# Performance work log

Hardware: AMD Instinct MI355X
Metric: run time of the kernel (lower is better)

## Reference

```python
import jax, jax.numpy as jnp
import numpy as np

N = 131072        # minibatch nodes
T = 100000        # rows per featured type table
D = 512           # raw feature dim for featured types
E = 256           # embedding size
NUM_NODES = 262144  # total nodes in graph (node embedding table rows)


def setup_inputs() -> dict:
    key = jax.random.key(0)
    ks = jax.random.split(key, 8)
    return {
        "node_ids": jax.random.randint(ks[0], (N,), 0, NUM_NODES),
        "node_tids": jax.random.randint(ks[1], (N,), 0, 4),
        "type_ids": jax.random.randint(ks[2], (N,), 0, T),
        "feats0": jax.random.normal(ks[3], (T, D), dtype=jnp.float32),
        "feats1": jax.random.normal(ks[4], (T, D), dtype=jnp.float32),
        "W0": jax.random.normal(ks[5], (D, E), dtype=jnp.float32) * (6.0 / (D + E)) ** 0.5,
        "W1": jax.random.normal(ks[6], (D, E), dtype=jnp.float32) * (6.0 / (D + E)) ** 0.5,
        "node_emb": jax.random.uniform(ks[7], (NUM_NODES, E), dtype=jnp.float32, minval=-1.0, maxval=1.0),
    }


def reference(node_ids, node_tids, type_ids, feats0, feats1, W0, W1, node_emb):
    # Per-type dispatch: types 0,1 have raw features projected by W_t;
    # types 2,3 read the learnable node-embedding table.
    m0 = (node_tids == 0)
    m1 = (node_tids == 1)
    # safe gather indices (masked-out rows read row 0, then zeroed)
    y0 = (feats0[jnp.where(m0, type_ids, 0)] @ W0) * m0[:, None].astype(W0.dtype)
    y1 = (feats1[jnp.where(m1, type_ids, 0)] @ W1) * m1[:, None].astype(W1.dtype)
    m_emb = jnp.logical_not(m0 | m1)
    ye = node_emb[node_ids] * m_emb[:, None].astype(node_emb.dtype)
    return y0 + y1 + ye  # [N, E]
```

## Files before the change

### kernel.cpp

```cpp
#include <hip/hip_runtime.h>
#include <hip/hip_bf16.h>

typedef __attribute__((ext_vector_type(4))) float f32x4;
typedef __attribute__((ext_vector_type(8))) short bf16x8;

#define NN 131072
#define TT 100000
#define DD 512
#define EE 256

__device__ inline ushort f2bf(float f) {
    union { float f; unsigned u; } x; x.f = f;
    unsigned r = x.u + 0x7fffu + ((x.u >> 16) & 1u);
    return (ushort)(r >> 16);
}

__global__ void compact_kernel(const int* __restrict__ tids, int* __restrict__ cnt,
                               int* __restrict__ l0, int* __restrict__ l1) {
    const int i = blockIdx.x * 256 + threadIdx.x;
    const int t = tids[i];
    const int lane = threadIdx.x & 63, wid = threadIdx.x >> 6;
    unsigned long long b0 = __ballot(t == 0);
    unsigned long long b1 = __ballot(t == 1);
    __shared__ int w0[4], w1[4];
    __shared__ int base0, base1;
    if (lane == 0) { w0[wid] = __popcll(b0); w1[wid] = __popcll(b1); }
    __syncthreads();
    if (threadIdx.x == 0) {
        base0 = atomicAdd(&cnt[0], w0[0] + w0[1] + w0[2] + w0[3]);
        base1 = atomicAdd(&cnt[1], w1[0] + w1[1] + w1[2] + w1[3]);
    }
    __syncthreads();
    int p0 = 0, p1 = 0;
#pragma unroll
    for (int w = 0; w < 4; ++w) if (w < wid) { p0 += w0[w]; p1 += w1[w]; }
    const unsigned long long ltm = (1ull << lane) - 1ull;
    if (t == 0)      l0[base0 + p0 + __popcll(b0 & ltm)] = i;
    else if (t == 1) l1[base1 + p1 + __popcll(b1 & ltm)] = i;
}

__global__ void prep_w_kernel(const float* __restrict__ W0, const float* __restrict__ W1,
                              ushort* __restrict__ Wt0, ushort* __restrict__ Wt1,
                              int* __restrict__ cnt) {
    if (blockIdx.x == 0 && threadIdx.x < 4) cnt[threadIdx.x] = 0;
    int gid = blockIdx.x * 256 + threadIdx.x;
    int t = gid >> 15;
    int rem = gid & 32767;
    int d = rem >> 6, eg = rem & 63;
    const float* W = t ? W1 : W0;
    ushort* Wt = t ? Wt1 : Wt0;
    f32x4 v = *(const f32x4*)(W + d * EE + eg * 4);
#pragma unroll
    for (int j = 0; j < 4; ++j)
        Wt[(size_t)(eg * 4 + j) * DD + d] = f2bf(v[j]);
}

__global__ void emb_gather_kernel(const int* __restrict__ ids, const int* __restrict__ tids,
                                  const float* __restrict__ emb, float* __restrict__ out) {
    int gid = blockIdx.x * 256 + threadIdx.x;
    int i = gid >> 6, j = gid & 63;
    if (tids[i] >= 2) {
        ((f32x4*)out)[(size_t)i * 64 + j] = ((const f32x4*)emb)[(size_t)ids[i] * 64 + j];
    }
}

__global__ __launch_bounds__(512, 4) void gemm_gather_kernel(
    const int* __restrict__ l0, const int* __restrict__ l1,
    const int* __restrict__ cntp, const int* __restrict__ type_ids,
    const float* __restrict__ feats0, const float* __restrict__ feats1,
    const ushort* __restrict__ Wt0, const ushort* __restrict__ Wt1,
    float* __restrict__ out) {
    const int cnt0 = cntp[0], cnt1 = cntp[1];
    const int ntile0 = (cnt0 + 127) >> 7;
    const int ntile1 = (cnt1 + 127) >> 7;
    const int b = blockIdx.x;
    const int* list; const float* feats; const ushort* Wt; int cnt, tile;
    if (b < ntile0)                { tile = b;          list = l0; feats = feats0; Wt = Wt0; cnt = cnt0; }
    else if (b < ntile0 + ntile1)  { tile = b - ntile0; list = l1; feats = feats1; Wt = Wt1; cnt = cnt1; }
    else return;
    const int row0 = tile * 128;

    __shared__ char Alds[128 * 64 * 2];
    __shared__ char Blds[256 * 64 * 2];

    const int tid = threadIdx.x;
    const int lane = tid & 63, wid = tid >> 6;
    const int wr = wid >> 1, wc = wid & 1;
    const int ln15 = lane & 15, lq = lane >> 4;

    const int ar = tid >> 2, aseg = tid & 3;
    const int rg = row0 + ar;
    int arow = 0;
    if (rg < cnt) arow = type_ids[list[rg]];
    const float* asrc = feats + (size_t)arow * DD + aseg * 16;
    int aw0 = ar * 128 + aseg * 32;
    int aw1 = aw0 + 16;
    aw0 ^= (ar & 7) << 4;
    aw1 ^= (ar & 7) << 4;

    f32x4 acc[2][8] = {};

    for (int k0 = 0; k0 < DD; k0 += 64) {
        const f32x4* ap = (const f32x4*)(asrc + k0);
        f32x4 v0 = ap[0], v1 = ap[1], v2 = ap[2], v3 = ap[3];
        bf16x8 h0, h1;
        h0[0] = (short)f2bf(v0[0]); h0[1] = (short)f2bf(v0[1]);
        h0[2] = (short)f2bf(v0[2]); h0[3] = (short)f2bf(v0[3]);
        h0[4] = (short)f2bf(v1[0]); h0[5] = (short)f2bf(v1[1]);
        h0[6] = (short)f2bf(v1[2]); h0[7] = (short)f2bf(v1[3]);
        h1[0] = (short)f2bf(v2[0]); h1[1] = (short)f2bf(v2[1]);
        h1[2] = (short)f2bf(v2[2]); h1[3] = (short)f2bf(v2[3]);
        h1[4] = (short)f2bf(v3[0]); h1[5] = (short)f2bf(v3[1]);
        h1[6] = (short)f2bf(v3[2]); h1[7] = (short)f2bf(v3[3]);
        *(bf16x8*)(Alds + aw0) = h0;
        *(bf16x8*)(Alds + aw1) = h1;

#pragma unroll
        for (int p = 0; p < 4; ++p) {
            int c = p * 512 + tid;
            int col = c >> 3, seg = c & 7;
            bf16x8 bv = *(const bf16x8*)(Wt + col * DD + k0 + seg * 8);
            int addr = col * 128 + seg * 16;
            addr ^= (col & 7) << 4;
            *(bf16x8*)(Blds + addr) = bv;
        }
        __syncthreads();

#pragma unroll
        for (int kh = 0; kh < 2; ++kh) {
            const int kb = kh * 64 + lq * 16;
            int ra0 = wr * 32 + ln15;
            int a0addr = (ra0 * 128 + kb) ^ ((ra0 & 7) << 4);
            int ra1 = ra0 + 16;
            int a1addr = (ra1 * 128 + kb) ^ ((ra1 & 7) << 4);
            bf16x8 a0 = *(const bf16x8*)(Alds + a0addr);
            bf16x8 a1 = *(const bf16x8*)(Alds + a1addr);
#pragma unroll
            for (int ni = 0; ni < 8; ++ni) {
                int col = wc * 128 + ni * 16 + ln15;
                int baddr = (col * 128 + kb) ^ ((col & 7) << 4);
                bf16x8 b = *(const bf16x8*)(Blds + baddr);
                acc[0][ni] = __builtin_amdgcn_mfma_f32_16x16x32_bf16(a0, b, acc[0][ni], 0, 0, 0);
                acc[1][ni] = __builtin_amdgcn_mfma_f32_16x16x32_bf16(a1, b, acc[1][ni], 0, 0, 0);
            }
        }
        __syncthreads();
    }

#pragma unroll
    for (int mi = 0; mi < 2; ++mi) {
        int mbase = row0 + wr * 32 + mi * 16 + lq * 4;
#pragma unroll
        for (int rr = 0; rr < 4; ++rr) {
            int r = mbase + rr;
            if (r < cnt) {
                int nd = list[r];
                float* orow = out + (size_t)nd * EE + wc * 128 + ln15;
#pragma unroll
                for (int ni = 0; ni < 8; ++ni) orow[ni * 16] = acc[mi][ni][rr];
            }
        }
    }
}

extern "C" void kernel_launch(void* const* d_in, const int* in_sizes, int n_in,
                              void* d_out, int out_size, void* d_ws, size_t ws_size,
                              hipStream_t stream) {
    const int*   node_ids  = (const int*)d_in[0];
    const int*   node_tids = (const int*)d_in[1];
    const int*   type_ids  = (const int*)d_in[2];
    const float* feats0    = (const float*)d_in[3];
    const float* feats1    = (const float*)d_in[4];
    const float* W0        = (const float*)d_in[5];
    const float* W1        = (const float*)d_in[6];
    const float* node_emb  = (const float*)d_in[7];
    float* out = (float*)d_out;

    char* ws = (char*)d_ws;
    int* cnt = (int*)ws;
    int* l0  = (int*)(ws + 16);
    int* l1  = (int*)(ws + 16 + 524288);
    ushort* Wt0 = (ushort*)(ws + 16 + 2 * 524288);
    ushort* Wt1 = Wt0 + DD * EE;

    prep_w_kernel<<<256, 256, 0, stream>>>(W0, W1, Wt0, Wt1, cnt);
    compact_kernel<<<512, 256, 0, stream>>>(node_tids, cnt, l0, l1);
    emb_gather_kernel<<<32768, 256, 0, stream>>>(node_ids, node_tids, node_emb, out);
    gemm_gather_kernel<<<2048, 512, 0, stream>>>(l0, l1, cnt, type_ids,
                                                 feats0, feats1, Wt0, Wt1, out);
}
```

Measured before the change: 130.1 us.

## Fuse embedding gather into GEMM kernel and prefetch next A tile

Merges the separate embedding-gather launch into the gather-GEMM kernel, with trailing blocks handling 32 embedding rows each, so one launch is removed and the memory-bound gather can overlap with the MFMA tiles. The GEMM k-loop is fully unrolled and the next 64-column slice of the feature row is loaded into registers before the current slice is converted and multiplied, hiding global-load latency. This costs more registers. Because the grid is sized NT_MAX + EMB_BLOCKS, gather blocks sit behind up to NT_MAX GEMM block indices and some idle blocks launch.

```diff
diff --git a/kernel.cpp b/kernel.cpp
--- a/kernel.cpp
+++ b/kernel.cpp
@@ -8,11 +8,29 @@
 #define TT 100000
 #define DD 512
 #define EE 256
+#define NT_MAX 1026
+#define EMB_BLOCKS 4096
 
 __device__ inline ushort f2bf(float f) {
     union { float f; unsigned u; } x; x.f = f;
     unsigned r = x.u + 0x7fffu + ((x.u >> 16) & 1u);
     return (ushort)(r >> 16);
+}
+
+__global__ void prep_w_kernel(const float* __restrict__ W0, const float* __restrict__ W1,
+                              ushort* __restrict__ Wt0, ushort* __restrict__ Wt1,
+                              int* __restrict__ cnt) {
+    if (blockIdx.x == 0 && threadIdx.x < 4) cnt[threadIdx.x] = 0;
+    int gid = blockIdx.x * 256 + threadIdx.x;
+    int t = gid >> 15;
+    int rem = gid & 32767;
+    int d = rem >> 6, eg = rem & 63;
+    const float* W = t ? W1 : W0;
+    ushort* Wt = t ? Wt1 : Wt0;
+    f32x4 v = *(const f32x4*)(W + d * EE + eg * 4);
+#pragma unroll
+    for (int j = 0; j < 4; ++j)
+        Wt[(size_t)(eg * 4 + j) * DD + d] = f2bf(v[j]);
 }
 
 __global__ void compact_kernel(const int* __restrict__ tids, int* __restrict__ cnt,
@@ -39,51 +57,42 @@
     else if (t == 1) l1[base1 + p1 + __popcll(b1 & ltm)] = i;
 }
 
-__global__ void prep_w_kernel(const float* __restrict__ W0, const float* __restrict__ W1,
-                              ushort* __restrict__ Wt0, ushort* __restrict__ Wt1,
-                              int* __restrict__ cnt) {
-    if (blockIdx.x == 0 && threadIdx.x < 4) cnt[threadIdx.x] = 0;
-    int gid = blockIdx.x * 256 + threadIdx.x;
-    int t = gid >> 15;
-    int rem = gid & 32767;
-    int d = rem >> 6, eg = rem & 63;
-    const float* W = t ? W1 : W0;
-    ushort* Wt = t ? Wt1 : Wt0;
-    f32x4 v = *(const f32x4*)(W + d * EE + eg * 4);
-#pragma unroll
-    for (int j = 0; j < 4; ++j)
-        Wt[(size_t)(eg * 4 + j) * DD + d] = f2bf(v[j]);
-}
-
-__global__ void emb_gather_kernel(const int* __restrict__ ids, const int* __restrict__ tids,
-                                  const float* __restrict__ emb, float* __restrict__ out) {
-    int gid = blockIdx.x * 256 + threadIdx.x;
-    int i = gid >> 6, j = gid & 63;
-    if (tids[i] >= 2) {
-        ((f32x4*)out)[(size_t)i * 64 + j] = ((const f32x4*)emb)[(size_t)ids[i] * 64 + j];
-    }
-}
-
-__global__ __launch_bounds__(512, 4) void gemm_gather_kernel(
+__global__ __launch_bounds__(512, 4) void mega_kernel(
     const int* __restrict__ l0, const int* __restrict__ l1,
     const int* __restrict__ cntp, const int* __restrict__ type_ids,
     const float* __restrict__ feats0, const float* __restrict__ feats1,
     const ushort* __restrict__ Wt0, const ushort* __restrict__ Wt1,
-    float* __restrict__ out) {
+    const int* __restrict__ node_ids, const int* __restrict__ node_tids,
+    const float* __restrict__ node_emb, float* __restrict__ out) {
     const int cnt0 = cntp[0], cnt1 = cntp[1];
-    const int ntile0 = (cnt0 + 127) >> 7;
-    const int ntile1 = (cnt1 + 127) >> 7;
+    const int nt0 = (cnt0 + 127) >> 7;
+    const int nt1 = (cnt1 + 127) >> 7;
+    const int nt = nt0 + nt1;
     const int b = blockIdx.x;
+    const int tid = threadIdx.x;
+
+    if (b >= nt) {
+        const int c = b - nt;
+        if (c >= EMB_BLOCKS) return;
+        const int wid = tid >> 6, lane = tid & 63;
+#pragma unroll
+        for (int it = 0; it < 4; ++it) {
+            const int row = c * 32 + it * 8 + wid;
+            if (node_tids[row] >= 2)
+                ((f32x4*)out)[(size_t)row * 64 + lane] =
+                    ((const f32x4*)node_emb)[(size_t)node_ids[row] * 64 + lane];
+        }
+        return;
+    }
+
     const int* list; const float* feats; const ushort* Wt; int cnt, tile;
-    if (b < ntile0)                { tile = b;          list = l0; feats = feats0; Wt = Wt0; cnt = cnt0; }
-    else if (b < ntile0 + ntile1)  { tile = b - ntile0; list = l1; feats = feats1; Wt = Wt1; cnt = cnt1; }
-    else return;
+    if (b < nt0) { tile = b;       list = l0; feats = feats0; Wt = Wt0; cnt = cnt0; }
+    else         { tile = b - nt0; list = l1; feats = feats1; Wt = Wt1; cnt = cnt1; }
     const int row0 = tile * 128;
 
     __shared__ char Alds[128 * 64 * 2];
     __shared__ char Blds[256 * 64 * 2];
 
-    const int tid = threadIdx.x;
     const int lane = tid & 63, wid = tid >> 6;
     const int wr = wid >> 1, wc = wid & 1;
     const int ln15 = lane & 15, lq = lane >> 4;
@@ -100,18 +109,27 @@
 
     f32x4 acc[2][8] = {};
 
-    for (int k0 = 0; k0 < DD; k0 += 64) {
-        const f32x4* ap = (const f32x4*)(asrc + k0);
-        f32x4 v0 = ap[0], v1 = ap[1], v2 = ap[2], v3 = ap[3];
+    f32x4 cur0, cur1, cur2, cur3;
+    { const f32x4* ap = (const f32x4*)asrc;
+      cur0 = ap[0]; cur1 = ap[1]; cur2 = ap[2]; cur3 = ap[3]; }
+
+#pragma unroll
+    for (int kk = 0; kk < 8; ++kk) {
+        const int k0 = kk * 64;
+        f32x4 nxt0, nxt1, nxt2, nxt3;
+        if (kk < 7) {
+            const f32x4* apn = (const f32x4*)(asrc + k0 + 64);
+            nxt0 = apn[0]; nxt1 = apn[1]; nxt2 = apn[2]; nxt3 = apn[3];
+        }
         bf16x8 h0, h1;
-        h0[0] = (short)f2bf(v0[0]); h0[1] = (short)f2bf(v0[1]);
-        h0[2] = (short)f2bf(v0[2]); h0[3] = (short)f2bf(v0[3]);
-        h0[4] = (short)f2bf(v1[0]); h0[5] = (short)f2bf(v1[1]);
-        h0[6] = (short)f2bf(v1[2]); h0[7] = (short)f2bf(v1[3]);
-        h1[0] = (short)f2bf(v2[0]); h1[1] = (short)f2bf(v2[1]);
-        h1[2] = (short)f2bf(v2[2]); h1[3] = (short)f2bf(v2[3]);
-        h1[4] = (short)f2bf(v3[0]); h1[5] = (short)f2bf(v3[1]);
-        h1[6] = (short)f2bf(v3[2]); h1[7] = (short)f2bf(v3[3]);
+        h0[0] = (short)f2bf(cur0[0]); h0[1] = (short)f2bf(cur0[1]);
+        h0[2] = (short)f2bf(cur0[2]); h0[3] = (short)f2bf(cur0[3]);
+        h0[4] = (short)f2bf(cur1[0]); h0[5] = (short)f2bf(cur1[1]);
+        h0[6] = (short)f2bf(cur1[2]); h0[7] = (short)f2bf(cur1[3]);
+        h1[0] = (short)f2bf(cur2[0]); h1[1] = (short)f2bf(cur2[1]);
+        h1[2] = (short)f2bf(cur2[2]); h1[3] = (short)f2bf(cur2[3]);
+        h1[4] = (short)f2bf(cur3[0]); h1[5] = (short)f2bf(cur3[1]);
+        h1[6] = (short)f2bf(cur3[2]); h1[7] = (short)f2bf(cur3[3]);
         *(bf16x8*)(Alds + aw0) = h0;
         *(bf16x8*)(Alds + aw1) = h1;
 
@@ -139,12 +157,14 @@
             for (int ni = 0; ni < 8; ++ni) {
                 int col = wc * 128 + ni * 16 + ln15;
                 int baddr = (col * 128 + kb) ^ ((col & 7) << 4);
-                bf16x8 b = *(const bf16x8*)(Blds + baddr);
-                acc[0][ni] = __builtin_amdgcn_mfma_f32_16x16x32_bf16(a0, b, acc[0][ni], 0, 0, 0);
-                acc[1][ni] = __builtin_amdgcn_mfma_f32_16x16x32_bf16(a1, b, acc[1][ni], 0, 0, 0);
+                bf16x8 bfr = *(const bf16x8*)(Blds + baddr);
+                acc[0][ni] = __builtin_amdgcn_mfma_f32_16x16x32_bf16(a0, bfr, acc[0][ni], 0, 0, 0);
+                acc[1][ni] = __builtin_amdgcn_mfma_f32_16x16x32_bf16(a1, bfr, acc[1][ni], 0, 0, 0);
             }
         }
         __syncthreads();
+
+        if (kk < 7) { cur0 = nxt0; cur1 = nxt1; cur2 = nxt2; cur3 = nxt3; }
     }
 
 #pragma unroll
@@ -185,7 +205,7 @@
 
     prep_w_kernel<<<256, 256, 0, stream>>>(W0, W1, Wt0, Wt1, cnt);
     compact_kernel<<<512, 256, 0, stream>>>(node_tids, cnt, l0, l1);
-    emb_gather_kernel<<<32768, 256, 0, stream>>>(node_ids, node_tids, node_emb, out);
-    gemm_gather_kernel<<<2048, 512, 0, stream>>>(l0, l1, cnt, type_ids,
-                                                 feats0, feats1, Wt0, Wt1, out);
-}
+    mega_kernel<<<NT_MAX + EMB_BLOCKS, 512, 0, stream>>>(
+        l0, l1, cnt, type_ids, feats0, feats1, Wt0, Wt1,
+        node_ids, node_tids, node_emb, out);
+}
```

New measurement: 144.1 us. 1.11x slower.
